# Optimization experiments

Measured on AMD Instinct MI355X. Metric: run time of the kernel, lower is better.

The kernel has to match this reference:

```python
import jax, jax.numpy as jnp
import numpy as np

D_MODEL, H, G = 2048, 32, 8
D_K = D_MODEL // H          # 64
GROUP_SIZE = H // G         # 4
B, S = 2, 2048


def setup_inputs() -> dict:
    key = jax.random.key(0)
    ks = jax.random.split(key, 9)
    sd = 1.0 / np.sqrt(D_MODEL)
    x = jax.random.normal(ks[0], (B, S, D_MODEL), dtype=jnp.float32)
    Wq = jax.random.normal(ks[1], (D_MODEL, D_MODEL), dtype=jnp.float32) * sd
    bq = jax.random.normal(ks[2], (D_MODEL,), dtype=jnp.float32) * 0.01
    Wk = jax.random.normal(ks[3], (D_MODEL, G * D_K), dtype=jnp.float32) * sd
    bk = jax.random.normal(ks[4], (G * D_K,), dtype=jnp.float32) * 0.01
    Wv = jax.random.normal(ks[5], (D_MODEL, G * D_K), dtype=jnp.float32) * sd
    bv = jax.random.normal(ks[6], (G * D_K,), dtype=jnp.float32) * 0.01
    Wo = jax.random.normal(ks[7], (D_MODEL, D_MODEL), dtype=jnp.float32) * sd
    bo = jax.random.normal(ks[8], (D_MODEL,), dtype=jnp.float32) * 0.01
    return {"x": x, "Wq": Wq, "bq": bq, "Wk": Wk, "bk": bk,
            "Wv": Wv, "bv": bv, "Wo": Wo, "bo": bo}


def reference(x, Wq, bq, Wk, bk, Wv, bv, Wo, bo):
    Bsz, Sln, _ = x.shape
    # projections
    Q = (x @ Wq + bq).reshape(Bsz, Sln, H, D_K).transpose(0, 2, 1, 3)   # [B,h,S,dk]
    K = (x @ Wk + bk).reshape(Bsz, Sln, G, D_K).transpose(0, 2, 1, 3)   # [B,g,S,dk]
    V = (x @ Wv + bv).reshape(Bsz, Sln, G, D_K).transpose(0, 2, 1, 3)   # [B,g,S,dk]
    # reshape Q into groups: [B, g, group_size, S, dk]; K/V broadcast over group dim
    Qg = Q.reshape(Bsz, G, GROUP_SIZE, Sln, D_K)
    scores = jnp.einsum('bgmqd,bgkd->bgmqk', Qg, K) / jnp.sqrt(jnp.float32(D_K))
    attn = jax.nn.softmax(scores, axis=-1)                              # [B,g,gs,S,S]
    out = jnp.einsum('bgmqk,bgkd->bgmqd', attn, V)                      # [B,g,gs,S,dk]
    out = out.reshape(Bsz, H, Sln, D_K).transpose(0, 2, 1, 3).reshape(Bsz, Sln, D_MODEL)
    return out @ Wo + bo
```

## Files before the change

### kernel.cpp

```cpp
#include <hip/hip_runtime.h>
#include <stdint.h>

#define DMODEL 2048
#define NHEADS 32
#define NGRP 8
#define DKH 64
#define BATCH 2
#define SEQ 2048
#define MTOT (BATCH*SEQ)

typedef unsigned short u16;
typedef __bf16 bf16x8 __attribute__((ext_vector_type(8)));
typedef float f32x4 __attribute__((ext_vector_type(4)));
typedef _Float16 f16x4 __attribute__((ext_vector_type(4)));
typedef _Float16 f16x8 __attribute__((ext_vector_type(8)));
typedef _Float16 f16x2 __attribute__((ext_vector_type(2)));

#define QSCALE 0.18033688011112042f

__device__ __forceinline__ u16 f2bf(float f){
    uint32_t x = __float_as_uint(f);
    x += 0x7FFFu + ((x >> 16) & 1u);
    return (u16)(x >> 16);
}

__device__ __forceinline__ void gld_lds16(const u16* g, u16* l){
    __builtin_amdgcn_global_load_lds(
        (const __attribute__((address_space(1))) uint32_t*)g,
        (__attribute__((address_space(3))) uint32_t*)l, 16, 0, 0);
}


__global__ void cvt_x_kern(const float* __restrict__ x, u16* __restrict__ xb){
    int i = (blockIdx.x * 256 + threadIdx.x) * 4;
    float4 v = *(const float4*)(x + i);
    uint32_t lo = (uint32_t)f2bf(v.x) | ((uint32_t)f2bf(v.y) << 16);
    uint32_t hi = (uint32_t)f2bf(v.z) | ((uint32_t)f2bf(v.w) << 16);
    *(uint2*)(xb + i) = make_uint2(lo, hi);
}

__global__ void cvt_wT_all(const float* __restrict__ Wq, const float* __restrict__ Wk,
                           const float* __restrict__ Wv, const float* __restrict__ Wo,
                           u16* __restrict__ WqT, u16* __restrict__ WkT,
                           u16* __restrict__ WvT, u16* __restrict__ WoT){
    __shared__ float t[32][33];
    int bx = blockIdx.x;
    const float* W; u16* T; int N; int cx;
    if (bx < 64)      { W = Wq; T = WqT; N = 2048; cx = bx; }
    else if (bx < 80) { W = Wk; T = WkT; N = 512;  cx = bx - 64; }
    else if (bx < 96) { W = Wv; T = WvT; N = 512;  cx = bx - 80; }
    else              { W = Wo; T = WoT; N = 2048; cx = bx - 96; }
    int tx = threadIdx.x & 31, ty = threadIdx.x >> 5;
    int n0 = cx * 32, k0 = blockIdx.y * 32;
#pragma unroll
    for (int i = 0; i < 4; i++)
        t[ty*4+i][tx] = W[(size_t)(k0 + ty*4 + i) * N + n0 + tx];
    __syncthreads();
#pragma unroll
    for (int i = 0; i < 4; i++)
        T[(size_t)(n0 + ty*4 + i) * DMODEL + k0 + tx] = f2bf(t[tx][ty*4+i]);
}

template<int EPI>
__global__ __launch_bounds__(256, 2) void gemm_nt(
    const u16* __restrict__ A, const u16* __restrict__ Bt,
    const float* __restrict__ bias0, const float* __restrict__ bias1, const float* __restrict__ bias2,
    void* __restrict__ out0, void* __restrict__ out1, void* __restrict__ out2, int Kn)
{
    __shared__ alignas(16) u16 As[128*32];
    __shared__ alignas(16) u16 Bs[128*32];
    const int tid  = threadIdx.x;
    const int w    = tid >> 6, lane = tid & 63, quad = lane >> 4, l16 = lane & 15;
    const int wr   = w >> 1,  wc   = w & 1;
    const int m0   = blockIdx.x * 128, n0 = blockIdx.y * 128;
    const int arow = lane >> 2, acol = (lane & 3) * 8;

    const u16* ga = A  + (size_t)(m0 + w*32 + arow) * Kn + acol;
    const u16* gb = Bt + (size_t)(n0 + w*32 + arow) * Kn + acol;
    u16* la = As + (w*32) * 32;
    u16* lb = Bs + (w*32) * 32;

    f32x4 acc[4][4] = {};

    for (int k0 = 0; k0 < Kn; k0 += 32){
        __syncthreads();
        gld_lds16(ga + k0,                  la);
        gld_lds16(ga + k0 + (size_t)16*Kn,  la + 16*32);
        gld_lds16(gb + k0,                  lb);
        gld_lds16(gb + k0 + (size_t)16*Kn,  lb + 16*32);
        __syncthreads();
        bf16x8 af[4], bfr[4];
#pragma unroll
        for (int t = 0; t < 4; t++)
            af[t]  = *(const bf16x8*)(As + (wr*64 + t*16 + l16)*32 + quad*8);
#pragma unroll
        for (int t = 0; t < 4; t++)
            bfr[t] = *(const bf16x8*)(Bs + (wc*64 + t*16 + l16)*32 + quad*8);
#pragma unroll
        for (int tm = 0; tm < 4; tm++)
#pragma unroll
            for (int tn = 0; tn < 4; tn++)
                acc[tm][tn] = __builtin_amdgcn_mfma_f32_16x16x32_bf16(af[tm], bfr[tn], acc[tm][tn], 0, 0, 0);
    }

#pragma unroll
    for (int tn = 0; tn < 4; tn++){
        int col = n0 + wc*64 + tn*16 + l16;
        float bv;
        if (EPI == 3) bv = (col < 2048) ? bias0[col] : (col < 2560) ? bias1[col-2048] : bias2[col-2560];
        else          bv = bias0[col];
#pragma unroll
        for (int tm = 0; tm < 4; tm++){
#pragma unroll
            for (int r = 0; r < 4; r++){
                int row = m0 + wr*64 + tm*16 + quad*4 + r;
                float v = acc[tm][tn][r] + bv;
                if (EPI == 3){
                    int b = row >> 11, s = row & (SEQ-1);
                    if (col < 2048){
                        int hh = col >> 6, d = col & 63;
                        ((u16*)out0)[(((size_t)b*NHEADS + hh)*SEQ + s)*DKH + d] = f2bf(v * QSCALE);
                    } else if (col < 2560){
                        int c = col - 2048, gg = c >> 6, d = c & 63;
                        ((u16*)out1)[(((size_t)b*NGRP + gg)*SEQ + s)*DKH + d] = f2bf(v);
                    } else {
                        int c = col - 2560, gg = c >> 6, d = c & 63;
                        int t = s & 31;
                        int pos = (t < 16) ? (((t >> 2) << 3) | (t & 3))
                                           : ((((t & 15) >> 2) << 3) | 4 | (t & 3));
                        int sp = (s & ~31) | pos;
                        ((u16*)out2)[(((size_t)b*NGRP + gg)*DKH + d)*SEQ + sp] =
                            __builtin_bit_cast(u16, (_Float16)v);
                    }
                } else {
                    ((float*)out0)[(size_t)row * DMODEL + col] = v;
                }
            }
        }
    }
}

__global__ __launch_bounds__(256, 4) void flash_kern(
    const u16* __restrict__ Qb, const u16* __restrict__ Kb,
    const u16* __restrict__ Vt, u16* __restrict__ Ob)
{
    __shared__ alignas(16) u16 Ks[2][64*64];
    __shared__ alignas(16) u16 Vs[2][64*64];
    const int tid = threadIdx.x, w = tid >> 6, lane = tid & 63;
    const int quad = lane >> 4, l16 = lane & 15;
    const int q0 = blockIdx.x * 128;
    const int h  = blockIdx.y, b = blockIdx.z, g = h >> 2;

    const u16* Qg = Qb + (((size_t)b*NHEADS + h)*SEQ + q0 + w*32) * DKH;
    const u16* Kg = Kb + ((size_t)b*NGRP + g) * SEQ * DKH;
    const u16* Vg = Vt + ((size_t)b*NGRP + g) * DKH * SEQ;

    const int lr = lane >> 3, lc = lane & 7;
    const int sw = lc ^ lr;
    const u16* gk0 = Kg + (size_t)(w*16 + lr) * DKH + sw*8;
    const u16* gv0 = Vg + (size_t)(w*16 + lr) * SEQ + sw*8;

    bf16x8 aq[2][2];
#pragma unroll
    for (int nt = 0; nt < 2; nt++)
#pragma unroll
        for (int ks = 0; ks < 2; ks++)
            aq[ks][nt] = *(const bf16x8*)(Qg + (nt*16 + l16)*DKH + ks*32 + quad*8);

    float lsum[2] = {};
    f32x4 oa[2][4] = {};

#define STAGE(buf, kt) do{                                                        \
        gld_lds16(gk0 + (size_t)(kt)*64*DKH,           Ks[buf] + (w*16)*64);      \
        gld_lds16(gk0 + (size_t)(kt)*64*DKH + 8*DKH,   Ks[buf] + (w*16+8)*64);    \
        gld_lds16(gv0 + (size_t)(kt)*64,               Vs[buf] + (w*16)*64);      \
        gld_lds16(gv0 + (size_t)(kt)*64 + (size_t)8*SEQ, Vs[buf] + (w*16+8)*64);  \
    }while(0)

#define COMPUTE(buf) do{                                                              \
        _Pragma("unroll")                                                             \
        for (int p = 0; p < 2; p++){                                                  \
            f16x4 pe[2], po[2];                                                       \
            _Pragma("unroll")                                                         \
            for (int hf = 0; hf < 2; hf++){                                           \
                const int kc = p*2 + hf;                                              \
                bf16x8 bk0 = *(const bf16x8*)(Ks[buf] + (kc*16 + l16)*64              \
                                              + ((quad     ^ (l16&7)) * 8));          \
                bf16x8 bk1 = *(const bf16x8*)(Ks[buf] + (kc*16 + l16)*64              \
                                              + (((4+quad) ^ (l16&7)) * 8));          \
                _Pragma("unroll")                                                     \
                for (int nt = 0; nt < 2; nt++){                                       \
                    f32x4 sa = {};                                                    \
                    sa = __builtin_amdgcn_mfma_f32_16x16x32_bf16(bk0, aq[0][nt], sa,0,0,0);\
                    sa = __builtin_amdgcn_mfma_f32_16x16x32_bf16(bk1, aq[1][nt], sa,0,0,0);\
                    float e0 = __builtin_amdgcn_exp2f(sa[0]);                         \
                    float e1 = __builtin_amdgcn_exp2f(sa[1]);                         \
                    float e2 = __builtin_amdgcn_exp2f(sa[2]);                         \
                    float e3 = __builtin_amdgcn_exp2f(sa[3]);                         \
                    lsum[nt] += (e0 + e1) + (e2 + e3);                                \
                    uint2 pk = make_uint2(                                            \
                        __builtin_bit_cast(uint32_t, __builtin_amdgcn_cvt_pkrtz(e0, e1)), \
                        __builtin_bit_cast(uint32_t, __builtin_amdgcn_cvt_pkrtz(e2, e3)));\
                    (hf ? po : pe)[nt] = __builtin_bit_cast(f16x4, pk);               \
                }                                                                     \
            }                                                                         \
            f16x8 pa8[2];                                                             \
            _Pragma("unroll")                                                         \
            for (int nt = 0; nt < 2; nt++)                                            \
                pa8[nt] = __builtin_shufflevector(pe[nt], po[nt], 0,1,2,3,4,5,6,7);   \
            _Pragma("unroll")                                                         \
            for (int dt = 0; dt < 4; dt++){                                           \
                f16x8 bv8 = *(const f16x8*)(Vs[buf] + (dt*16 + l16)*64                \
                             + (((4*p + quad) ^ (l16&7)) * 8));                       \
                _Pragma("unroll")                                                     \
                for (int nt = 0; nt < 2; nt++)                                        \
                    oa[nt][dt] = __builtin_amdgcn_mfma_f32_16x16x32_f16(              \
                        pa8[nt], bv8, oa[nt][dt], 0, 0, 0);                           \
            }                                                                         \
        }                                                                             \
    }while(0)

    STAGE(0, 0);
    __syncthreads();

    for (int kt2 = 0; kt2 < SEQ/128; ++kt2){
        int kt = kt2 * 2;
        STAGE(1, kt + 1);
        COMPUTE(0);
        __syncthreads();
        if (kt2 < SEQ/128 - 1) STAGE(0, kt + 2);
        COMPUTE(1);
        __syncthreads();
    }

#pragma unroll
    for (int nt = 0; nt < 2; nt++){
        float s = lsum[nt];
        s += __shfl_xor(s, 16, 64);
        s += __shfl_xor(s, 32, 64);
        lsum[nt] = 1.0f / s;
    }

#pragma unroll
    for (int nt = 0; nt < 2; nt++)
#pragma unroll
        for (int r = 0; r < 4; r++){
            float inv = __shfl(lsum[nt], quad*4 + r, 64);
            int q = q0 + w*32 + nt*16 + quad*4 + r;
#pragma unroll
            for (int dt = 0; dt < 4; dt++)
                Ob[((size_t)b*SEQ + q)*DMODEL + h*DKH + dt*16 + l16] = f2bf(oa[nt][dt][r] * inv);
        }
#undef STAGE
#undef COMPUTE
}


extern "C" void kernel_launch(void* const* d_in, const int* in_sizes, int n_in,
                              void* d_out, int out_size, void* d_ws, size_t ws_size,
                              hipStream_t stream)
{
    const float* x  = (const float*)d_in[0];
    const float* Wq = (const float*)d_in[1];
    const float* bq = (const float*)d_in[2];
    const float* Wk = (const float*)d_in[3];
    const float* bk = (const float*)d_in[4];
    const float* Wv = (const float*)d_in[5];
    const float* bv = (const float*)d_in[6];
    const float* Wo = (const float*)d_in[7];
    const float* bo = (const float*)d_in[8];

    uint8_t* p = (uint8_t*)d_ws;
    u16* xb  = (u16*)p; p += (size_t)MTOT*DMODEL*2;
    u16* WqT = (u16*)p; p += (size_t)DMODEL*DMODEL*2;
    u16* WkT = (u16*)p; p += (size_t)(NGRP*DKH)*DMODEL*2;
    u16* WvT = (u16*)p; p += (size_t)(NGRP*DKH)*DMODEL*2;
    u16* WoT = (u16*)p; p += (size_t)DMODEL*DMODEL*2;
    u16* Qb  = (u16*)p; p += (size_t)BATCH*NHEADS*SEQ*DKH*2;
    u16* Kb  = (u16*)p; p += (size_t)BATCH*NGRP*SEQ*DKH*2;
    u16* Vtb = (u16*)p; p += (size_t)BATCH*NGRP*DKH*SEQ*2;
    u16* Ob  = (u16*)p; p += (size_t)MTOT*DMODEL*2;

    cvt_x_kern<<<MTOT*DMODEL/1024, 256, 0, stream>>>(x, xb);
    cvt_wT_all<<<dim3(160, 64), 256, 0, stream>>>(Wq, Wk, Wv, Wo, WqT, WkT, WvT, WoT);

    gemm_nt<3><<<dim3(MTOT/128, 3072/128), 256, 0, stream>>>(
        xb, WqT, bq, bk, bv, Qb, Kb, Vtb, DMODEL);

    flash_kern<<<dim3(SEQ/128, NHEADS, BATCH), 256, 0, stream>>>(Qb, Kb, Vtb, Ob);

    gemm_nt<2><<<dim3(MTOT/128, DMODEL/128), 256, 0, stream>>>(
        Ob, WoT, bo, nullptr, nullptr, d_out, nullptr, nullptr, DMODEL);
}
```

Baseline: 316.7 us.

## Replace GEMM with 256x256 tile, 4-stage LDS pipeline, swizzle and XCD remap

The projection GEMMs move from a 128x128 single-buffered tile with 4 waves to a 256x256 tile with 8 waves. Global-to-LDS loads run through a 4-slot ring buffer with explicit vmcnt waits, so loads overlap the MFMA work. The LDS layout is XOR-swizzled to avoid bank conflicts, MFMA sections are wrapped in s_setprio, and block IDs are remapped across the 8 XCDs for cache locality. The risks are a hardcoded K loop (assumes Kn=2048), heavy register pressure from 32 accumulators per wave, and much larger LDS use, which cuts occupancy.

```diff
diff --git a/kernel.cpp b/kernel.cpp
--- a/kernel.cpp
+++ b/kernel.cpp
@@ -14,7 +14,6 @@
 typedef float f32x4 __attribute__((ext_vector_type(4)));
 typedef _Float16 f16x4 __attribute__((ext_vector_type(4)));
 typedef _Float16 f16x8 __attribute__((ext_vector_type(8)));
-typedef _Float16 f16x2 __attribute__((ext_vector_type(2)));
 
 #define QSCALE 0.18033688011112042f
 
@@ -62,59 +61,110 @@
 }
 
 template<int EPI>
-__global__ __launch_bounds__(256, 2) void gemm_nt(
+__global__ __launch_bounds__(512, 2) void gemm_nt8(
     const u16* __restrict__ A, const u16* __restrict__ Bt,
     const float* __restrict__ bias0, const float* __restrict__ bias1, const float* __restrict__ bias2,
     void* __restrict__ out0, void* __restrict__ out1, void* __restrict__ out2, int Kn)
 {
-    __shared__ alignas(16) u16 As[128*32];
-    __shared__ alignas(16) u16 Bs[128*32];
-    const int tid  = threadIdx.x;
-    const int w    = tid >> 6, lane = tid & 63, quad = lane >> 4, l16 = lane & 15;
-    const int wr   = w >> 1,  wc   = w & 1;
-    const int m0   = blockIdx.x * 128, n0 = blockIdx.y * 128;
-    const int arow = lane >> 2, acol = (lane & 3) * 8;
-
-    const u16* ga = A  + (size_t)(m0 + w*32 + arow) * Kn + acol;
-    const u16* gb = Bt + (size_t)(n0 + w*32 + arow) * Kn + acol;
-    u16* la = As + (w*32) * 32;
-    u16* lb = Bs + (w*32) * 32;
-
-    f32x4 acc[4][4] = {};
-
-    for (int k0 = 0; k0 < Kn; k0 += 32){
-        __syncthreads();
-        gld_lds16(ga + k0,                  la);
-        gld_lds16(ga + k0 + (size_t)16*Kn,  la + 16*32);
-        gld_lds16(gb + k0,                  lb);
-        gld_lds16(gb + k0 + (size_t)16*Kn,  lb + 16*32);
-        __syncthreads();
-        bf16x8 af[4], bfr[4];
-#pragma unroll
-        for (int t = 0; t < 4; t++)
-            af[t]  = *(const bf16x8*)(As + (wr*64 + t*16 + l16)*32 + quad*8);
-#pragma unroll
-        for (int t = 0; t < 4; t++)
-            bfr[t] = *(const bf16x8*)(Bs + (wc*64 + t*16 + l16)*32 + quad*8);
-#pragma unroll
-        for (int tm = 0; tm < 4; tm++)
-#pragma unroll
-            for (int tn = 0; tn < 4; tn++)
-                acc[tm][tn] = __builtin_amdgcn_mfma_f32_16x16x32_bf16(af[tm], bfr[tn], acc[tm][tn], 0, 0, 0);
+    __shared__ alignas(16) u16 Asub[4][8192];
+    __shared__ alignas(16) u16 Bsub[4][8192];
+    const int tid = threadIdx.x, w = tid >> 6, lane = tid & 63;
+    const int quad = lane >> 4, l16 = lane & 15;
+    const int wm = w >> 2, wn = w & 3;
+
+    int bid = blockIdx.y * gridDim.x + blockIdx.x;
+    int nwg = gridDim.x * gridDim.y;
+    int cpx = nwg >> 3;
+    int sbid = (bid & 7) * cpx + (bid >> 3);
+    int bx = sbid % gridDim.x, by = sbid / gridDim.x;
+    const int m0 = bx * 256, n0 = by * 256;
+
+    const int srow = w*16 + (lane >> 2);
+    const int sc   = lane & 3;
+    const int gc   = sc ^ ((srow >> 1) & 3);
+    const u16* gA = A  + (size_t)(m0 + srow) * Kn + gc*8;
+    const u16* gB = Bt + (size_t)(n0 + srow) * Kn + gc*8;
+
+    const int swc = (quad ^ ((l16 >> 1) & 3)) * 8;
+
+    bf16x8 af[8], bfr[2];
+    f32x4 acc[8][4] = {};
+
+#define STGA(slot, kk) do{ \
+        gld_lds16(gA + (kk),                  &Asub[slot][w*512]); \
+        gld_lds16(gA + (kk) + (size_t)128*Kn, &Asub[slot][4096 + w*512]); }while(0)
+#define STGB(slot, kk) do{ \
+        gld_lds16(gB + (kk),                  &Bsub[slot][w*512]); \
+        gld_lds16(gB + (kk) + (size_t)128*Kn, &Bsub[slot][4096 + w*512]); }while(0)
+
+#define W_LG  asm volatile("s_waitcnt lgkmcnt(0)" ::: "memory")
+#define W_VM8 asm volatile("s_waitcnt vmcnt(8) lgkmcnt(0)" ::: "memory")
+#define W_VM4 asm volatile("s_waitcnt vmcnt(4) lgkmcnt(0)" ::: "memory")
+#define W_VM0 asm volatile("s_waitcnt vmcnt(0) lgkmcnt(0)" ::: "memory")
+
+#define PHASE(slot, nh, STG_STMT, WAIT) do{                                          \
+        if (nh == 0){                                                                \
+            _Pragma("unroll")                                                        \
+            for (int m = 0; m < 8; m++)                                              \
+                af[m] = *(const bf16x8*)(&Asub[slot][(wm*128 + m*16 + l16)*32 + swc]); \
+        }                                                                            \
+        _Pragma("unroll")                                                            \
+        for (int nl = 0; nl < 2; nl++)                                               \
+            bfr[nl] = *(const bf16x8*)(&Bsub[slot][(wn*64 + ((nh)*2+nl)*16 + l16)*32 + swc]); \
+        STG_STMT;                                                                    \
+        WAIT;                                                                        \
+        __syncthreads();                                                             \
+        __builtin_amdgcn_s_setprio(1);                                               \
+        _Pragma("unroll")                                                            \
+        for (int m = 0; m < 8; m++){                                                 \
+            acc[m][(nh)*2+0] = __builtin_amdgcn_mfma_f32_16x16x32_bf16(af[m], bfr[0], acc[m][(nh)*2+0], 0,0,0); \
+            acc[m][(nh)*2+1] = __builtin_amdgcn_mfma_f32_16x16x32_bf16(af[m], bfr[1], acc[m][(nh)*2+1], 0,0,0); \
+        }                                                                            \
+        __builtin_amdgcn_s_setprio(0);                                               \
+    }while(0)
+
+    STGA(0, 0);  STGB(0, 0);
+    STGA(1, 32); STGB(1, 32);
+    STGA(2, 64); STGB(2, 64);
+    asm volatile("s_waitcnt vmcnt(8)" ::: "memory");
+    __syncthreads();
+
+    for (int j = 0; j < 15; j++){
+        const int kb = 128*j;
+        PHASE(0, 0, STGA(3, kb+96),  W_LG);
+        PHASE(0, 1, STGB(3, kb+96),  W_VM8);
+        PHASE(1, 0, STGA(0, kb+128), W_LG);
+        PHASE(1, 1, STGB(0, kb+128), W_VM8);
+        PHASE(2, 0, STGA(1, kb+160), W_LG);
+        PHASE(2, 1, STGB(1, kb+160), W_VM8);
+        PHASE(3, 0, STGA(2, kb+192), W_LG);
+        PHASE(3, 1, STGB(2, kb+192), W_VM8);
     }
-
-#pragma unroll
-    for (int tn = 0; tn < 4; tn++){
-        int col = n0 + wc*64 + tn*16 + l16;
+    PHASE(0, 0, STGA(3, 2016), W_LG);
+    PHASE(0, 1, STGB(3, 2016), W_VM8);
+    PHASE(1, 0, (void)0,       W_LG);
+    PHASE(1, 1, (void)0,       W_VM4);
+    PHASE(2, 0, (void)0,       W_LG);
+    PHASE(2, 1, (void)0,       W_VM0);
+    PHASE(3, 0, (void)0,       W_LG);
+    PHASE(3, 1, (void)0,       W_LG);
+
+#undef PHASE
+#undef STGA
+#undef STGB
+
+#pragma unroll
+    for (int n = 0; n < 4; n++){
+        int col = n0 + wn*64 + n*16 + l16;
         float bv;
         if (EPI == 3) bv = (col < 2048) ? bias0[col] : (col < 2560) ? bias1[col-2048] : bias2[col-2560];
         else          bv = bias0[col];
 #pragma unroll
-        for (int tm = 0; tm < 4; tm++){
+        for (int m = 0; m < 8; m++){
 #pragma unroll
             for (int r = 0; r < 4; r++){
-                int row = m0 + wr*64 + tm*16 + quad*4 + r;
-                float v = acc[tm][tn][r] + bv;
+                int row = m0 + wm*128 + m*16 + quad*4 + r;
+                float v = acc[m][n][r] + bv;
                 if (EPI == 3){
                     int b = row >> 11, s = row & (SEQ-1);
                     if (col < 2048){
@@ -284,11 +334,11 @@
     cvt_x_kern<<<MTOT*DMODEL/1024, 256, 0, stream>>>(x, xb);
     cvt_wT_all<<<dim3(160, 64), 256, 0, stream>>>(Wq, Wk, Wv, Wo, WqT, WkT, WvT, WoT);
 
-    gemm_nt<3><<<dim3(MTOT/128, 3072/128), 256, 0, stream>>>(
+    gemm_nt8<3><<<dim3(MTOT/256, 3072/256), 512, 0, stream>>>(
         xb, WqT, bq, bk, bv, Qb, Kb, Vtb, DMODEL);
 
     flash_kern<<<dim3(SEQ/128, NHEADS, BATCH), 256, 0, stream>>>(Qb, Kb, Vtb, Ob);
 
-    gemm_nt<2><<<dim3(MTOT/128, DMODEL/128), 256, 0, stream>>>(
+    gemm_nt8<2><<<dim3(MTOT/256, DMODEL/256), 512, 0, stream>>>(
         Ob, WoT, bo, nullptr, nullptr, d_out, nullptr, nullptr, DMODEL);
 }
```

After: 377.8 us. 1.19x slower.

## Add 256x256 eight-wave pipelined GEMM for fused QKV projection

Applied to the files above, without the earlier changes.

Introduces gemm_nt8, a 512-thread kernel computing 256x256 output tiles with double-buffered LDS staging via global_load_lds. It interleaves prefetch of future K-slices with MFMA phases, XOR-swizzles LDS columns to reduce bank conflicts, and remaps block IDs across eight groups for cache locality. The QKV projection now uses it, while the output projection keeps the old kernel. This trades more registers and LDS per block and a hand-tuned barrier and waitcnt schedule for better data reuse and load/compute overlap.

```diff
diff --git a/kernel.cpp b/kernel.cpp
--- a/kernel.cpp
+++ b/kernel.cpp
@@ -14,7 +14,6 @@
 typedef float f32x4 __attribute__((ext_vector_type(4)));
 typedef _Float16 f16x4 __attribute__((ext_vector_type(4)));
 typedef _Float16 f16x8 __attribute__((ext_vector_type(8)));
-typedef _Float16 f16x2 __attribute__((ext_vector_type(2)));
 
 #define QSCALE 0.18033688011112042f
 
@@ -62,59 +61,106 @@
 }
 
 template<int EPI>
-__global__ __launch_bounds__(256, 2) void gemm_nt(
+__global__ __launch_bounds__(512, 2) void gemm_nt8(
     const u16* __restrict__ A, const u16* __restrict__ Bt,
     const float* __restrict__ bias0, const float* __restrict__ bias1, const float* __restrict__ bias2,
     void* __restrict__ out0, void* __restrict__ out1, void* __restrict__ out2, int Kn)
 {
-    __shared__ alignas(16) u16 As[128*32];
-    __shared__ alignas(16) u16 Bs[128*32];
-    const int tid  = threadIdx.x;
-    const int w    = tid >> 6, lane = tid & 63, quad = lane >> 4, l16 = lane & 15;
-    const int wr   = w >> 1,  wc   = w & 1;
-    const int m0   = blockIdx.x * 128, n0 = blockIdx.y * 128;
-    const int arow = lane >> 2, acol = (lane & 3) * 8;
-
-    const u16* ga = A  + (size_t)(m0 + w*32 + arow) * Kn + acol;
-    const u16* gb = Bt + (size_t)(n0 + w*32 + arow) * Kn + acol;
-    u16* la = As + (w*32) * 32;
-    u16* lb = Bs + (w*32) * 32;
-
-    f32x4 acc[4][4] = {};
-
-    for (int k0 = 0; k0 < Kn; k0 += 32){
-        __syncthreads();
-        gld_lds16(ga + k0,                  la);
-        gld_lds16(ga + k0 + (size_t)16*Kn,  la + 16*32);
-        gld_lds16(gb + k0,                  lb);
-        gld_lds16(gb + k0 + (size_t)16*Kn,  lb + 16*32);
-        __syncthreads();
-        bf16x8 af[4], bfr[4];
-#pragma unroll
-        for (int t = 0; t < 4; t++)
-            af[t]  = *(const bf16x8*)(As + (wr*64 + t*16 + l16)*32 + quad*8);
-#pragma unroll
-        for (int t = 0; t < 4; t++)
-            bfr[t] = *(const bf16x8*)(Bs + (wc*64 + t*16 + l16)*32 + quad*8);
-#pragma unroll
-        for (int tm = 0; tm < 4; tm++)
-#pragma unroll
-            for (int tn = 0; tn < 4; tn++)
-                acc[tm][tn] = __builtin_amdgcn_mfma_f32_16x16x32_bf16(af[tm], bfr[tn], acc[tm][tn], 0, 0, 0);
-    }
-
-#pragma unroll
-    for (int tn = 0; tn < 4; tn++){
-        int col = n0 + wc*64 + tn*16 + l16;
+    __shared__ alignas(16) u16 Asub[2][2][8192];
+    __shared__ alignas(16) u16 Bsub[2][2][8192];
+    const int tid = threadIdx.x, w = tid >> 6, lane = tid & 63;
+    const int quad = lane >> 4, l16 = lane & 15;
+    const int wm = w >> 2, wn = w & 3;
+
+    int bid = blockIdx.y * gridDim.x + blockIdx.x;
+    int nwg = gridDim.x * gridDim.y;
+    int cpx = nwg >> 3;
+    int sbid = (bid & 7) * cpx + (bid >> 3);
+    int bx = sbid % gridDim.x, by = sbid / gridDim.x;
+    const int m0 = bx * 256, n0 = by * 256;
+
+    const u16* gAw = A  + (size_t)(m0 + w*32 + (lane >> 2)) * Kn + (((lane&3) ^ ((lane>>3)&3)) * 8);
+    const u16* gBw = Bt + (size_t)(n0 + w*32 + (lane >> 2)) * Kn + (((lane&3) ^ ((lane>>3)&3)) * 8);
+
+    const int swc = (quad ^ ((l16 >> 1) & 3)) * 8;
+
+    bf16x8 af[8], bfr[2];
+    f32x4 acc[8][4] = {};
+
+#define SA(buf, kk, kt) do{ \
+        gld_lds16(gAw + (kt)*64 + (kk)*32,                   &Asub[buf][kk][w*1024]);       \
+        gld_lds16(gAw + (size_t)16*Kn + (kt)*64 + (kk)*32,   &Asub[buf][kk][w*1024 + 512]); \
+    }while(0)
+#define SB(buf, kk, kt) do{ \
+        gld_lds16(gBw + (kt)*64 + (kk)*32,                   &Bsub[buf][kk][w*1024]);       \
+        gld_lds16(gBw + (size_t)16*Kn + (kt)*64 + (kk)*32,   &Bsub[buf][kk][w*1024 + 512]); \
+    }while(0)
+
+#define NW  ((void)0)
+#define VM4 asm volatile("s_waitcnt vmcnt(4)" ::: "memory")
+
+#define PH(buf, np, kk, STG, WAIT) do{                                               \
+        if (np == 0){                                                                \
+            _Pragma("unroll")                                                        \
+            for (int m = 0; m < 8; m++)                                              \
+                af[m] = *(const bf16x8*)(&Asub[buf][kk][(wm*128 + m*16 + l16)*32 + swc]); \
+        }                                                                            \
+        _Pragma("unroll")                                                            \
+        for (int nl = 0; nl < 2; nl++)                                               \
+            bfr[nl] = *(const bf16x8*)(&Bsub[buf][kk][(wn*64 + ((np)*2+nl)*16 + l16)*32 + swc]); \
+        STG;                                                                         \
+        WAIT;                                                                        \
+        __builtin_amdgcn_s_barrier();                                                \
+        asm volatile("s_waitcnt lgkmcnt(0)" ::: "memory");                           \
+        __builtin_amdgcn_sched_barrier(0);                                           \
+        __builtin_amdgcn_s_setprio(1);                                               \
+        _Pragma("unroll")                                                            \
+        for (int m = 0; m < 8; m++){                                                 \
+            acc[m][(np)*2+0] = __builtin_amdgcn_mfma_f32_16x16x32_bf16(af[m], bfr[0], acc[m][(np)*2+0], 0,0,0); \
+            acc[m][(np)*2+1] = __builtin_amdgcn_mfma_f32_16x16x32_bf16(af[m], bfr[1], acc[m][(np)*2+1], 0,0,0); \
+        }                                                                            \
+        __builtin_amdgcn_s_setprio(0);                                               \
+        __builtin_amdgcn_s_barrier();                                                \
+    }while(0)
+
+    SA(0, 0, 0); SB(0, 0, 0);
+    SA(0, 1, 0); SB(0, 1, 0);
+    SA(1, 0, 1); SB(1, 0, 1);
+    asm volatile("s_waitcnt vmcnt(4)" ::: "memory");
+    __builtin_amdgcn_s_barrier();
+
+    for (int j = 0; j < 16; j++){
+        const int tb = 2*j + 1;
+        const int tc = (2*j + 2 < 32) ? 2*j + 2 : 31;
+        const int td = (2*j + 3 < 32) ? 2*j + 3 : 31;
+        PH(0, 0, 0, SA(1, 1, tb), NW);
+        PH(0, 1, 0, SB(1, 1, tb), NW);
+        PH(0, 0, 1, SA(0, 0, tc), NW);
+        PH(0, 1, 1, SB(0, 0, tc), VM4);
+        PH(1, 0, 0, SA(0, 1, tc), NW);
+        PH(1, 1, 0, SB(0, 1, tc), NW);
+        PH(1, 0, 1, SA(1, 0, td), NW);
+        PH(1, 1, 1, SB(1, 0, td), VM4);
+    }
+
+#undef PH
+#undef SA
+#undef SB
+#undef NW
+#undef VM4
+
+#pragma unroll
+    for (int n = 0; n < 4; n++){
+        int col = n0 + wn*64 + n*16 + l16;
         float bv;
         if (EPI == 3) bv = (col < 2048) ? bias0[col] : (col < 2560) ? bias1[col-2048] : bias2[col-2560];
         else          bv = bias0[col];
 #pragma unroll
-        for (int tm = 0; tm < 4; tm++){
+        for (int m = 0; m < 8; m++){
 #pragma unroll
             for (int r = 0; r < 4; r++){
-                int row = m0 + wr*64 + tm*16 + quad*4 + r;
-                float v = acc[tm][tn][r] + bv;
+                int row = m0 + wm*128 + m*16 + quad*4 + r;
+                float v = acc[m][n][r] + bv;
                 if (EPI == 3){
                     int b = row >> 11, s = row & (SEQ-1);
                     if (col < 2048){
@@ -135,6 +181,64 @@
                 } else {
                     ((float*)out0)[(size_t)row * DMODEL + col] = v;
                 }
+            }
+        }
+    }
+}
+
+template<int EPI>
+__global__ __launch_bounds__(256, 2) void gemm_nt(
+    const u16* __restrict__ A, const u16* __restrict__ Bt,
+    const float* __restrict__ bias0, const float* __restrict__ bias1, const float* __restrict__ bias2,
+    void* __restrict__ out0, void* __restrict__ out1, void* __restrict__ out2, int Kn)
+{
+    __shared__ alignas(16) u16 As[128*32];
+    __shared__ alignas(16) u16 Bs[128*32];
+    const int tid  = threadIdx.x;
+    const int w    = tid >> 6, lane = tid & 63, quad = lane >> 4, l16 = lane & 15;
+    const int wr   = w >> 1,  wc   = w & 1;
+    const int m0   = blockIdx.x * 128, n0 = blockIdx.y * 128;
+    const int arow = lane >> 2, acol = (lane & 3) * 8;
+
+    const u16* ga = A  + (size_t)(m0 + w*32 + arow) * Kn + acol;
+    const u16* gb = Bt + (size_t)(n0 + w*32 + arow) * Kn + acol;
+    u16* la = As + (w*32) * 32;
+    u16* lb = Bs + (w*32) * 32;
+
+    f32x4 acc[4][4] = {};
+
+    for (int k0 = 0; k0 < Kn; k0 += 32){
+        __syncthreads();
+        gld_lds16(ga + k0,                  la);
+        gld_lds16(ga + k0 + (size_t)16*Kn,  la + 16*32);
+        gld_lds16(gb + k0,                  lb);
+        gld_lds16(gb + k0 + (size_t)16*Kn,  lb + 16*32);
+        __syncthreads();
+        bf16x8 af[4], bfr[4];
+#pragma unroll
+        for (int t = 0; t < 4; t++)
+            af[t]  = *(const bf16x8*)(As + (wr*64 + t*16 + l16)*32 + quad*8);
+#pragma unroll
+        for (int t = 0; t < 4; t++)
+            bfr[t] = *(const bf16x8*)(Bs + (wc*64 + t*16 + l16)*32 + quad*8);
+#pragma unroll
+        for (int tm = 0; tm < 4; tm++)
+#pragma unroll
+            for (int tn = 0; tn < 4; tn++)
+                acc[tm][tn] = __builtin_amdgcn_mfma_f32_16x16x32_bf16(af[tm], bfr[tn], acc[tm][tn], 0, 0, 0);
+    }
+
+#pragma unroll
+    for (int tn = 0; tn < 4; tn++){
+        int col = n0 + wc*64 + tn*16 + l16;
+        float bv = bias0[col];
+#pragma unroll
+        for (int tm = 0; tm < 4; tm++){
+#pragma unroll
+            for (int r = 0; r < 4; r++){
+                int row = m0 + wr*64 + tm*16 + quad*4 + r;
+                float v = acc[tm][tn][r] + bv;
+                ((float*)out0)[(size_t)row * DMODEL + col] = v;
             }
         }
     }
@@ -284,7 +388,7 @@
     cvt_x_kern<<<MTOT*DMODEL/1024, 256, 0, stream>>>(x, xb);
     cvt_wT_all<<<dim3(160, 64), 256, 0, stream>>>(Wq, Wk, Wv, Wo, WqT, WkT, WvT, WoT);
 
-    gemm_nt<3><<<dim3(MTOT/128, 3072/128), 256, 0, stream>>>(
+    gemm_nt8<3><<<dim3(MTOT/256, 3072/256), 512, 0, stream>>>(
         xb, WqT, bq, bk, bv, Qb, Kb, Vtb, DMODEL);
 
     flash_kern<<<dim3(SEQ/128, NHEADS, BATCH), 256, 0, stream>>>(Qb, Kb, Vtb, Ob);
```

Result: slower. 330.6 us (+4.4%).
